# Performance work log

Measured on AMD Instinct MI355X. Metric: run time of the kernel, lower is better.

Reference implementation:

```python
import jax, jax.numpy as jnp
import numpy as np
import math

B, T, C = 2, 8192, 1024
H = 16
HD = C // H  # 64
WIN = 256    # local_window_size


def _rope_tables(T, hd):
    inv_freq = 1.0 / (10000.0 ** (np.arange(0, hd, 2, dtype=np.float32) / hd))
    t = np.arange(T, dtype=np.float32)
    freqs = np.outer(t, inv_freq)                      # [T, hd/2]
    emb = np.concatenate([freqs, freqs], axis=-1)      # [T, hd]
    return jnp.asarray(np.cos(emb))[None, None], jnp.asarray(np.sin(emb))[None, None]


def setup_inputs() -> dict:
    key = jax.random.key(0)
    ks = jax.random.split(key, 10)
    x = jax.random.normal(ks[0], (B, T, C), dtype=jnp.float32)
    # padding_mask: bool [B,T]; per the source, True positions end up masked out of attention
    padding_mask = jax.random.randint(ks[1], (B, T), 0, 2).astype(bool)
    cos, sin = _rope_tables(T, HD)                     # [1,1,T,HD]
    s = 1.0 / math.sqrt(C)
    Wq = jax.random.normal(ks[2], (C, C), dtype=jnp.float32) * s
    bq = jnp.zeros((C,), dtype=jnp.float32)
    Wk = jax.random.normal(ks[3], (C, C), dtype=jnp.float32) * s
    bk = jnp.zeros((C,), dtype=jnp.float32)
    Wv = jax.random.normal(ks[4], (C, C), dtype=jnp.float32) * s
    bv = jnp.zeros((C,), dtype=jnp.float32)
    Wo = jax.random.normal(ks[5], (C, C), dtype=jnp.float32) * s
    bo = jnp.zeros((C,), dtype=jnp.float32)
    return {"x": x, "padding_mask": padding_mask, "cos": cos, "sin": sin,
            "Wq": Wq, "bq": bq, "Wk": Wk, "bk": bk, "Wv": Wv, "bv": bv,
            "Wo": Wo, "bo": bo}


def _rotate_half(t):
    h = t.shape[-1] // 2
    return jnp.concatenate([-t[..., h:], t[..., :h]], axis=-1)


def reference(x, padding_mask, cos, sin, Wq, bq, Wk, bk, Wv, bv, Wo, bo):
    Bx, Tx, Cx = x.shape
    Wn = WIN
    pad_end = (Wn - Tx % Wn) % Wn            # static python int
    Tp = Tx + pad_end
    nW = Tp // Wn
    half = Wn // 2
    hd = cos.shape[-1]

    cos_t = jnp.broadcast_to(cos[0, 0][None], (Bx, Tx, hd))
    sin_t = jnp.broadcast_to(sin[0, 0][None], (Bx, Tx, hd))
    if pad_end > 0:
        x = jnp.pad(x, ((0, 0), (0, pad_end), (0, 0)))
        padding_mask = jnp.pad(padding_mask, ((0, 0), (0, pad_end)))
        cos_t = jnp.pad(cos_t, ((0, 0), (0, pad_end), (0, 0)))
        sin_t = jnp.pad(sin_t, ((0, 0), (0, pad_end), (0, 0)))

    # non-overlapping query windows: [B*nW, W, C]
    q_win = x.reshape(Bx * nW, Wn, Cx)
    cos_q = cos_t.reshape(Bx * nW, Wn, hd)[:, None]   # [Bw,1,W,hd]
    sin_q = sin_t.reshape(Bx * nW, Wn, hd)[:, None]

    # overlapping key/value windows of size 2W, stride W
    x_ctx = jnp.pad(x, ((0, 0), (half, half), (0, 0)))
    cos_ctx = jnp.pad(cos_t, ((0, 0), (half, half), (0, 0)))
    sin_ctx = jnp.pad(sin_t, ((0, 0), (half, half), (0, 0)))
    pk = jnp.pad(padding_mask, ((0, 0), (half, half)))  # pad value False
    idx = jnp.arange(nW)[:, None] * Wn + jnp.arange(2 * Wn)[None, :]  # [nW, 2W]
    k_win = x_ctx[:, idx].reshape(Bx * nW, 2 * Wn, Cx)
    cos_k = cos_ctx[:, idx].reshape(Bx * nW, 2 * Wn, hd)[:, None]
    sin_k = sin_ctx[:, idx].reshape(Bx * nW, 2 * Wn, hd)[:, None]
    pk = pk[:, idx].reshape(Bx * nW, 2 * Wn)

    # attn_mask: True = attend (SDPA bool-mask convention)
    attn_mask = ~pk
    all_attend = jnp.all(attn_mask, axis=-1)
    attn_mask = attn_mask.at[:, 0].set(jnp.where(all_attend, False, attn_mask[:, 0]))

    Bw = Bx * nW
    q = (q_win @ Wq.T + bq).reshape(Bw, Wn, H, HD).transpose(0, 2, 1, 3)        # [Bw,H,W,hd]
    k = (k_win @ Wk.T + bk).reshape(Bw, 2 * Wn, H, HD).transpose(0, 2, 1, 3)    # [Bw,H,2W,hd]
    v = (k_win @ Wv.T + bv).reshape(Bw, 2 * Wn, H, HD).transpose(0, 2, 1, 3)

    q = q * cos_q + _rotate_half(q) * sin_q
    k = k * cos_k + _rotate_half(k) * sin_k

    scale = 1.0 / math.sqrt(HD)
    scores = jnp.einsum('bhqd,bhkd->bhqk', q, k) * scale                        # [Bw,H,W,2W]
    scores = jnp.where(attn_mask[:, None, None, :], scores, jnp.finfo(scores.dtype).min)
    attn = jax.nn.softmax(scores, axis=-1)
    out = jnp.einsum('bhqk,bhkd->bhqd', attn, v)
    out = out.transpose(0, 2, 1, 3).reshape(Bw, Wn, Cx)
    out = out @ Wo.T + bo
    out = out.reshape(Bx, nW * Wn, Cx)[:, :Tx]
    return out
```

## Files before the change

kernel.cpp:

```cpp
#include <hip/hip_runtime.h>
#include <hip/hip_bf16.h>
#include <stdint.h>

#define T_SEQ 8192
#define B_SZ 2
#define CDIM 1024
#define NH 16
#define HDIM 64
#define NW 32

typedef unsigned short ushort_t;
typedef __attribute__((ext_vector_type(8))) short short8;
typedef __attribute__((ext_vector_type(8))) unsigned short us8;
typedef __attribute__((ext_vector_type(4))) unsigned short us4;
typedef __attribute__((ext_vector_type(4))) float f32x4;

__device__ __forceinline__ unsigned short f2bf(float f) {
  union { float f; unsigned int u; } c; c.f = f;
  return (unsigned short)((c.u + 0x7FFFu + ((c.u >> 16) & 1u)) >> 16);
}
__device__ __forceinline__ unsigned pk2(float a, float b) {
  unsigned r;
  asm("v_cvt_pk_bf16_f32 %0, %1, %2" : "=v"(r) : "v"(a), "v"(b));
  return r;
}
__device__ __forceinline__ void gld16(void* lds, const void* g) {
  __builtin_amdgcn_global_load_lds(
      (const __attribute__((address_space(1))) void*)g,
      (__attribute__((address_space(3))) void*)lds, 16, 0, 0);
}

__global__ __launch_bounds__(256) void cvt_f32_bf16(const float* __restrict__ src,
                                                    ushort_t* __restrict__ dst, int n4)
{
  int i = blockIdx.x * 256 + threadIdx.x;
  if (i < n4) {
    float4 v = ((const float4*)src)[i];
    ushort4 o;
    o.x = f2bf(v.x); o.y = f2bf(v.y); o.z = f2bf(v.z); o.w = f2bf(v.w);
    ((ushort4*)dst)[i] = o;
  }
}

__global__ __launch_bounds__(256) void cvt_w4(const float* __restrict__ w0,
                                              const float* __restrict__ w1,
                                              const float* __restrict__ w2,
                                              const float* __restrict__ w3,
                                              ushort_t* __restrict__ dst)
{
  const float* srcs[4] = {w0, w1, w2, w3};
  const float* s = srcs[blockIdx.y];
  ushort_t* d = dst + (size_t)blockIdx.y * CDIM * CDIM;
  int i = blockIdx.x * 256 + threadIdx.x;
  float4 v = ((const float4*)s)[i];
  ushort4 o;
  o.x = f2bf(v.x); o.y = f2bf(v.y); o.z = f2bf(v.z); o.w = f2bf(v.w);
  ((ushort4*)d)[i] = o;
}

__device__ __forceinline__ void gemm_core(const ushort_t* __restrict__ A,
                                          const ushort_t* __restrict__ W,
                                          ushort_t* As, ushort_t* Bs,
                                          int m0, int n0, int t, f32x4 acc[4][4])
{
  const int lane = t & 63;
  const int wv = t >> 6;
  const int wm = (wv >> 1) * 64;
  const int wn = (wv & 1) * 64;
  const int fr = lane & 15;
  const int quad = lane >> 4;

  const int srow = t >> 3;
  const int sc8 = ((t & 7) ^ (srow & 7)) * 8;
  const ushort_t* Ag = A + (size_t)(m0 + srow) * CDIM + sc8;
  const ushort_t* Wg = W + (size_t)(n0 + srow) * CDIM + sc8;
  ushort_t* lA = &As[srow * 64 + (t & 7) * 8];
  ushort_t* lB = &Bs[srow * 64 + (t & 7) * 8];

  for (int kt = 0; kt < CDIM; kt += 64) {
    __syncthreads();
#pragma unroll
    for (int p = 0; p < 4; p++) gld16(lA + p * 2048, Ag + (size_t)p * 32 * CDIM + kt);
#pragma unroll
    for (int p = 0; p < 4; p++) gld16(lB + p * 2048, Wg + (size_t)p * 32 * CDIM + kt);
    __syncthreads();
#pragma unroll
    for (int ks = 0; ks < 2; ks++) {
      short8 a[4], b[4];
#pragma unroll
      for (int i = 0; i < 4; i++)
        a[i] = *(const short8*)&As[(wm + i * 16 + fr) * 64 + (((ks * 4 + quad) ^ (fr & 7)) * 8)];
#pragma unroll
      for (int j = 0; j < 4; j++)
        b[j] = *(const short8*)&Bs[(wn + j * 16 + fr) * 64 + (((ks * 4 + quad) ^ (fr & 7)) * 8)];
#pragma unroll
      for (int i = 0; i < 4; i++)
#pragma unroll
        for (int j = 0; j < 4; j++)
          acc[i][j] = __builtin_amdgcn_mfma_f32_16x16x32_bf16(a[i], b[j], acc[i][j], 0, 0, 0);
    }
  }
}

__global__ __launch_bounds__(256, 4) void gemm_qkv(const ushort_t* __restrict__ A,
                                                   const ushort_t* __restrict__ Wcat,
                                                   const float* __restrict__ bq,
                                                   const float* __restrict__ bk,
                                                   const float* __restrict__ bv,
                                                   ushort_t* __restrict__ Qb,
                                                   ushort_t* __restrict__ Kb,
                                                   ushort_t* __restrict__ Vtb,
                                                   const float* __restrict__ cosT,
                                                   const float* __restrict__ sinT)
{
  __shared__ ushort_t SH[17408];
  ushort_t* As = SH;
  ushort_t* Bs = SH + 8192;

  const int t = threadIdx.x;
  const int lane = t & 63;
  const int wv = t >> 6;
  const int wm = (wv >> 1) * 64;
  const int wn = (wv & 1) * 64;
  const int fr = lane & 15;
  const int quad = lane >> 4;
  const int m0 = blockIdx.y * 128;
  const int n0 = blockIdx.x * 128;
  const int sec = blockIdx.x >> 3;
  const int nsec0 = (blockIdx.x & 7) * 128;
  const float* bias = (sec == 0) ? bq : (sec == 1) ? bk : bv;

  f32x4 acc[4][4];
#pragma unroll
  for (int i = 0; i < 4; i++)
#pragma unroll
    for (int j = 0; j < 4; j++) acc[i][j] = (f32x4){0.f, 0.f, 0.f, 0.f};

  gemm_core(A, Wcat, As, Bs, m0, n0, t, acc);

  __syncthreads();

  if (sec < 2) {
    ushort_t* OutQK = sec ? Kb : Qb;
#pragma unroll
    for (int jp = 0; jp < 2; jp++) {
      int d = jp * 16 + fr;
      int cl = wn + jp * 16 + fr;
      float bl = bias[nsec0 + cl];
      float bh = bias[nsec0 + cl + 32];
#pragma unroll
      for (int i = 0; i < 4; i++) {
        int rloc = wm + i * 16 + quad * 4;
#pragma unroll
        for (int r = 0; r < 4; r++) {
          int tt = (m0 + rloc + r) & (T_SEQ - 1);
          float c = cosT[tt * HDIM + d];
          float sn = sinT[tt * HDIM + d];
          float lo = acc[i][jp][r] + bl;
          float hi = acc[i][jp + 2][r] + bh;
          SH[(rloc + r) * 136 + cl] = f2bf(lo * c - hi * sn);
          SH[(rloc + r) * 136 + cl + 32] = f2bf(hi * c + lo * sn);
        }
      }
    }
    __syncthreads();
    const int rr0 = t >> 4;
    const int c8 = (t & 15) * 8;
    size_t gbase = (size_t)m0 * CDIM + nsec0 + c8;
#pragma unroll
    for (int p = 0; p < 8; p++) {
      int rr = p * 16 + rr0;
      *(us8*)&OutQK[gbase + (size_t)rr * CDIM] = *(const us8*)&SH[rr * 136 + c8];
    }
  } else {
#pragma unroll
    for (int j = 0; j < 4; j++) {
      int ch = nsec0 + wn + j * 16 + fr;
      float bvv = bias[ch];
#pragma unroll
      for (int i = 0; i < 4; i++) {
        int m = m0 + wm + i * 16 + quad * 4;
        int bb = m >> 13;
        int tq = m & (T_SEQ - 1);
        us4 pk;
#pragma unroll
        for (int r = 0; r < 4; r++) pk[r] = f2bf(acc[i][j][r] + bvv);
        *(us4*)&Vtb[((size_t)bb * CDIM + ch) * T_SEQ + tq] = pk;
      }
    }
  }
}

__global__ __launch_bounds__(256, 4) void gemm_out(const ushort_t* __restrict__ A,
                                                   const ushort_t* __restrict__ W,
                                                   const float* __restrict__ bias,
                                                   float* __restrict__ Out)
{
  __shared__ ushort_t SH[16384];
  ushort_t* As = SH;
  ushort_t* Bs = SH + 8192;

  const int t = threadIdx.x;
  const int lane = t & 63;
  const int wv = t >> 6;
  const int wm = (wv >> 1) * 64;
  const int wn = (wv & 1) * 64;
  const int fr = lane & 15;
  const int quad = lane >> 4;
  const int m0 = blockIdx.y * 128;
  const int n0 = blockIdx.x * 128;

  f32x4 acc[4][4];
#pragma unroll
  for (int i = 0; i < 4; i++)
#pragma unroll
    for (int j = 0; j < 4; j++) acc[i][j] = (f32x4){0.f, 0.f, 0.f, 0.f};

  gemm_core(A, W, As, Bs, m0, n0, t, acc);

#pragma unroll
  for (int j = 0; j < 4; j++) {
    int n = n0 + wn + j * 16 + fr;
    float bvv = bias[n];
#pragma unroll
    for (int i = 0; i < 4; i++) {
      int m = m0 + wm + i * 16 + quad * 4;
#pragma unroll
      for (int r = 0; r < 4; r++)
        Out[(size_t)(m + r) * CDIM + n] = acc[i][j][r] + bvv;
    }
  }
}

__global__ __launch_bounds__(256, 4) void attn_kernel(const ushort_t* __restrict__ Q,
                                                      const ushort_t* __restrict__ Kg,
                                                      const ushort_t* __restrict__ Vt,
                                                      const int* __restrict__ mask,
                                                      ushort_t* __restrict__ AO)
{
  __shared__ ushort_t Ks[64 * 72];
  __shared__ ushort_t Vts[64 * 72];
  __shared__ unsigned int PsW[4 * 32 * 32];
  __shared__ float attf[512];

  const int t = threadIdx.x;
  const int lane = t & 63;
  const int wv = t >> 6;
  const int h = blockIdx.x;
  const int w = blockIdx.y >> 1;
  const int qh = blockIdx.y & 1;
  const int b = blockIdx.z;
  const int fr = lane & 15;
  const int quad = lane >> 4;

  {
    int p0 = w * 256 + t - 128;
    bool a0 = (p0 < 0 || p0 >= T_SEQ) ? true : (mask[b * T_SEQ + p0] == 0);
    int p1 = p0 + 256;
    bool a1 = (p1 < 0 || p1 >= T_SEQ) ? true : (mask[b * T_SEQ + p1] == 0);
    int all1 = __syncthreads_and((int)(a0 && a1));
    attf[t] = a0 ? 0.f : -1.0e38f;
    attf[t + 256] = a1 ? 0.f : -1.0e38f;
    if (all1 && t == 0) attf[0] = -1.0e38f;
  }

  short8 qf[2][2];
  {
    const ushort_t* qp = Q + ((size_t)b * T_SEQ + w * 256 + qh * 128 + wv * 32 + fr) * CDIM
                           + h * HDIM + quad * 8;
#pragma unroll
    for (int mt = 0; mt < 2; mt++)
#pragma unroll
      for (int ks = 0; ks < 2; ks++)
        qf[mt][ks] = *(const short8*)&qp[(size_t)mt * 16 * CDIM + ks * 32];
  }

  const int srow = t >> 3;
  const int sc8 = (t & 7) * 8;
  const ushort_t* kgb = Kg + (size_t)b * T_SEQ * CDIM + h * HDIM + sc8;
  const ushort_t* vt_base = Vt + ((size_t)b * CDIM + h * HDIM) * T_SEQ;
  const float SCL = 0.18033688011112042f;

  unsigned int* pw = &PsW[wv * 1024];
  const int swz = (fr & 7) << 2;
  const int rbase = quad << 2;

  float m_run[2], l_run[2];
  f32x4 o[2][4];
#pragma unroll
  for (int mt = 0; mt < 2; mt++) { m_run[mt] = -3.0e38f; l_run[mt] = 0.f; }
#pragma unroll
  for (int mt = 0; mt < 2; mt++)
#pragma unroll
    for (int nt = 0; nt < 4; nt++) o[mt][nt] = (f32x4){0.f, 0.f, 0.f, 0.f};

  for (int kc = 0; kc < 8; kc++) {
    __syncthreads();
    {
#pragma unroll
      for (int p = 0; p < 2; p++) {
        int jj = p * 32 + srow;
        int pos = w * 256 + kc * 64 + jj - 128;
        us8 kval = (us8)(0);
        if (pos >= 0 && pos < T_SEQ) kval = *(const us8*)&kgb[(size_t)pos * CDIM];
        *(us8*)&Ks[jj * 72 + sc8] = kval;
      }
      int pos0 = w * 256 + kc * 64 - 128 + sc8;
      bool inr = (pos0 >= 0) && (pos0 < T_SEQ);
#pragma unroll
      for (int p = 0; p < 2; p++) {
        int d = p * 32 + srow;
        us8 vv = (us8)(0);
        if (inr) vv = *(const us8*)&vt_base[(size_t)d * T_SEQ + pos0];
        *(us8*)&Vts[d * 72 + sc8] = vv;
      }
    }
    __syncthreads();

    short8 kf[4][2];
#pragma unroll
    for (int nt = 0; nt < 4; nt++)
#pragma unroll
      for (int ks = 0; ks < 2; ks++)
        kf[nt][ks] = *(const short8*)&Ks[(nt * 16 + fr) * 72 + ks * 32 + quad * 8];

    f32x4 st[2][4];
#pragma unroll
    for (int mt = 0; mt < 2; mt++)
#pragma unroll
      for (int nt = 0; nt < 4; nt++) {
        f32x4 a = (f32x4){0.f, 0.f, 0.f, 0.f};
        a = __builtin_amdgcn_mfma_f32_16x16x32_bf16(kf[nt][0], qf[mt][0], a, 0, 0, 0);
        a = __builtin_amdgcn_mfma_f32_16x16x32_bf16(kf[nt][1], qf[mt][1], a, 0, 0, 0);
        st[mt][nt] = a;
      }

    f32x4 kb[4];
#pragma unroll
    for (int nt = 0; nt < 4; nt++)
      kb[nt] = *(const f32x4*)&attf[kc * 64 + nt * 16 + quad * 4];
#pragma unroll
    for (int mt = 0; mt < 2; mt++)
#pragma unroll
      for (int nt = 0; nt < 4; nt++)
#pragma unroll
        for (int r = 0; r < 4; r++)
          st[mt][nt][r] = __builtin_fmaf(st[mt][nt][r], SCL, kb[nt][r]);

#pragma unroll
    for (int mt = 0; mt < 2; mt++) {
      float t0 = fmaxf(fmaxf(st[mt][0][0], st[mt][0][1]), fmaxf(st[mt][0][2], st[mt][0][3]));
      float t1 = fmaxf(fmaxf(st[mt][1][0], st[mt][1][1]), fmaxf(st[mt][1][2], st[mt][1][3]));
      float t2 = fmaxf(fmaxf(st[mt][2][0], st[mt][2][1]), fmaxf(st[mt][2][2], st[mt][2][3]));
      float t3 = fmaxf(fmaxf(st[mt][3][0], st[mt][3][1]), fmaxf(st[mt][3][2], st[mt][3][3]));
      float mx = fmaxf(fmaxf(t0, t1), fmaxf(t2, t3));
      mx = fmaxf(mx, __shfl_xor(mx, 16, 64));
      mx = fmaxf(mx, __shfl_xor(mx, 32, 64));
      if (!__all(mx <= m_run[mt] + 8.f)) {
        float mnew = fmaxf(m_run[mt], mx);
        float alpha = __builtin_amdgcn_exp2f(m_run[mt] - mnew);
        m_run[mt] = mnew;
        l_run[mt] *= alpha;
        float af[4];
#pragma unroll
        for (int r = 0; r < 4; r++) af[r] = __shfl(alpha, rbase + r, 64);
#pragma unroll
        for (int nt = 0; nt < 4; nt++)
#pragma unroll
          for (int r = 0; r < 4; r++) o[mt][nt][r] *= af[r];
      }
      float rs = 0.f;
#pragma unroll
      for (int nt = 0; nt < 4; nt++)
#pragma unroll
        for (int r = 0; r < 4; r++) {
          float p = __builtin_amdgcn_exp2f(st[mt][nt][r] - m_run[mt]);
          st[mt][nt][r] = p;
          rs += p;
        }
      rs += __shfl_xor(rs, 16, 64);
      rs += __shfl_xor(rs, 32, 64);
      l_run[mt] += rs;

      unsigned int* pr = pw + ((mt * 16 + fr) << 5);
#pragma unroll
      for (int nt = 0; nt < 4; nt++)
#pragma unroll
        for (int hh = 0; hh < 2; hh++)
          pr[(((nt << 3) + (quad << 1) + hh)) ^ swz] =
              pk2(st[mt][nt][2 * hh], st[mt][nt][2 * hh + 1]);
    }

    short8 vf[4][2];
#pragma unroll
    for (int nt = 0; nt < 4; nt++)
#pragma unroll
      for (int ks = 0; ks < 2; ks++)
        vf[nt][ks] = *(const short8*)&Vts[(nt * 16 + fr) * 72 + ks * 32 + quad * 8];

#pragma unroll
    for (int mt = 0; mt < 2; mt++) {
      const unsigned int* pr = pw + ((mt * 16 + fr) << 5);
      short8 pf[2];
#pragma unroll
      for (int ks = 0; ks < 2; ks++)
        pf[ks] = *(const short8*)&pr[((ks << 4) + (quad << 2)) ^ swz];
#pragma unroll
      for (int nt = 0; nt < 4; nt++) {
        o[mt][nt] = __builtin_amdgcn_mfma_f32_16x16x32_bf16(pf[0], vf[nt][0], o[mt][nt], 0, 0, 0);
        o[mt][nt] = __builtin_amdgcn_mfma_f32_16x16x32_bf16(pf[1], vf[nt][1], o[mt][nt], 0, 0, 0);
      }
    }
  }

  size_t obase = ((size_t)b * T_SEQ + w * 256 + qh * 128 + wv * 32) * CDIM + h * HDIM;
#pragma unroll
  for (int mt = 0; mt < 2; mt++)
#pragma unroll
    for (int r = 0; r < 4; r++) {
      float lv = __shfl(l_run[mt], rbase + r, 64);
      float iv = 1.0f / fmaxf(lv, 1e-30f);
      int row = mt * 16 + quad * 4 + r;
#pragma unroll
      for (int nt = 0; nt < 4; nt++)
        AO[obase + (size_t)row * CDIM + nt * 16 + fr] = f2bf(o[mt][nt][r] * iv);
    }
}

extern "C" void kernel_launch(void* const* d_in, const int* in_sizes, int n_in,
                              void* d_out, int out_size, void* d_ws, size_t ws_size,
                              hipStream_t stream)
{
  const float* x    = (const float*)d_in[0];
  const int*   pm   = (const int*)d_in[1];
  const float* cosT = (const float*)d_in[2];
  const float* sinT = (const float*)d_in[3];
  const float* Wq   = (const float*)d_in[4];
  const float* bq   = (const float*)d_in[5];
  const float* Wk   = (const float*)d_in[6];
  const float* bk   = (const float*)d_in[7];
  const float* Wv   = (const float*)d_in[8];
  const float* bv   = (const float*)d_in[9];
  const float* Wo   = (const float*)d_in[10];
  const float* bo   = (const float*)d_in[11];
  float* out = (float*)d_out;

  const size_t NTOK = (size_t)B_SZ * T_SEQ;
  const size_t NELT = NTOK * CDIM;
  ushort_t* Kb  = (ushort_t*)d_out;
  ushort_t* xbf = (ushort_t*)d_out + NELT;
  char* ws = (char*)d_ws;
  ushort_t* Wbf = (ushort_t*)ws;
  ushort_t* Qb  = (ushort_t*)(ws + 4 * (size_t)CDIM * CDIM * 2);
  ushort_t* Vtb = Qb + NELT;
  ushort_t* AO  = Qb;

  cvt_f32_bf16<<<(int)(NELT / 4 / 256), 256, 0, stream>>>(x, xbf, (int)(NELT / 4));
  cvt_w4<<<dim3(CDIM * CDIM / 4 / 256, 4), 256, 0, stream>>>(Wq, Wk, Wv, Wo, Wbf);

  gemm_qkv<<<dim3(24, (int)(NTOK / 128)), 256, 0, stream>>>(
      xbf, Wbf, bq, bk, bv, Qb, Kb, Vtb, cosT, sinT);

  attn_kernel<<<dim3(NH, NW * 2, B_SZ), 256, 0, stream>>>(Qb, Kb, Vtb, pm, AO);

  gemm_out<<<dim3(8, (int)(NTOK / 128)), 256, 0, stream>>>(
      AO, Wbf + 3 * (size_t)CDIM * CDIM, bo, out);
}
```

Baseline: 420.8 us.

## Use 512-thread attention blocks per window to share K/V tiles across all queries

Each attention block now covers a whole 256-query window with 8 waves instead of splitting it across two 256-thread blocks. This halves the global loads of K/V into shared memory and the mask setup per window, since each thread loads one row instead of two. The P scratch buffer per wave shrinks because P is written and consumed per m-tile, and s_setprio is wrapped around the MFMA sections to favour matrix issue. The change also halves the grid size and raises per-block register and LDS pressure under the new launch bounds.

```diff
diff --git a/kernel.cpp b/kernel.cpp
--- a/kernel.cpp
+++ b/kernel.cpp
@@ -232,7 +232,7 @@
   }
 }
 
-__global__ __launch_bounds__(256, 4) void attn_kernel(const ushort_t* __restrict__ Q,
+__global__ __launch_bounds__(512, 8) void attn_kernel(const ushort_t* __restrict__ Q,
                                                       const ushort_t* __restrict__ Kg,
                                                       const ushort_t* __restrict__ Vt,
                                                       const int* __restrict__ mask,
@@ -240,33 +240,29 @@
 {
   __shared__ ushort_t Ks[64 * 72];
   __shared__ ushort_t Vts[64 * 72];
-  __shared__ unsigned int PsW[4 * 32 * 32];
+  __shared__ unsigned int PsW[8 * 16 * 32];
   __shared__ float attf[512];
 
   const int t = threadIdx.x;
   const int lane = t & 63;
   const int wv = t >> 6;
   const int h = blockIdx.x;
-  const int w = blockIdx.y >> 1;
-  const int qh = blockIdx.y & 1;
+  const int w = blockIdx.y;
   const int b = blockIdx.z;
   const int fr = lane & 15;
   const int quad = lane >> 4;
 
   {
     int p0 = w * 256 + t - 128;
-    bool a0 = (p0 < 0 || p0 >= T_SEQ) ? true : (mask[b * T_SEQ + p0] == 0);
-    int p1 = p0 + 256;
-    bool a1 = (p1 < 0 || p1 >= T_SEQ) ? true : (mask[b * T_SEQ + p1] == 0);
-    int all1 = __syncthreads_and((int)(a0 && a1));
-    attf[t] = a0 ? 0.f : -1.0e38f;
-    attf[t + 256] = a1 ? 0.f : -1.0e38f;
+    bool a = (p0 < 0 || p0 >= T_SEQ) ? true : (mask[b * T_SEQ + p0] == 0);
+    int all1 = __syncthreads_and((int)a);
+    attf[t] = a ? 0.f : -1.0e38f;
     if (all1 && t == 0) attf[0] = -1.0e38f;
   }
 
   short8 qf[2][2];
   {
-    const ushort_t* qp = Q + ((size_t)b * T_SEQ + w * 256 + qh * 128 + wv * 32 + fr) * CDIM
+    const ushort_t* qp = Q + ((size_t)b * T_SEQ + w * 256 + wv * 32 + fr) * CDIM
                            + h * HDIM + quad * 8;
 #pragma unroll
     for (int mt = 0; mt < 2; mt++)
@@ -281,7 +277,7 @@
   const ushort_t* vt_base = Vt + ((size_t)b * CDIM + h * HDIM) * T_SEQ;
   const float SCL = 0.18033688011112042f;
 
-  unsigned int* pw = &PsW[wv * 1024];
+  unsigned int* pw = &PsW[wv * 512];
   const int swz = (fr & 7) << 2;
   const int rbase = quad << 2;
 
@@ -297,23 +293,15 @@
   for (int kc = 0; kc < 8; kc++) {
     __syncthreads();
     {
-#pragma unroll
-      for (int p = 0; p < 2; p++) {
-        int jj = p * 32 + srow;
-        int pos = w * 256 + kc * 64 + jj - 128;
-        us8 kval = (us8)(0);
-        if (pos >= 0 && pos < T_SEQ) kval = *(const us8*)&kgb[(size_t)pos * CDIM];
-        *(us8*)&Ks[jj * 72 + sc8] = kval;
-      }
+      int pos = w * 256 + kc * 64 + srow - 128;
+      us8 kval = (us8)(0);
+      if (pos >= 0 && pos < T_SEQ) kval = *(const us8*)&kgb[(size_t)pos * CDIM];
+      *(us8*)&Ks[srow * 72 + sc8] = kval;
+
       int pos0 = w * 256 + kc * 64 - 128 + sc8;
-      bool inr = (pos0 >= 0) && (pos0 < T_SEQ);
-#pragma unroll
-      for (int p = 0; p < 2; p++) {
-        int d = p * 32 + srow;
-        us8 vv = (us8)(0);
-        if (inr) vv = *(const us8*)&vt_base[(size_t)d * T_SEQ + pos0];
-        *(us8*)&Vts[d * 72 + sc8] = vv;
-      }
+      us8 vv = (us8)(0);
+      if (pos0 >= 0 && pos0 < T_SEQ) vv = *(const us8*)&vt_base[(size_t)srow * T_SEQ + pos0];
+      *(us8*)&Vts[srow * 72 + sc8] = vv;
     }
     __syncthreads();
 
@@ -325,6 +313,7 @@
         kf[nt][ks] = *(const short8*)&Ks[(nt * 16 + fr) * 72 + ks * 32 + quad * 8];
 
     f32x4 st[2][4];
+    __builtin_amdgcn_s_setprio(1);
 #pragma unroll
     for (int mt = 0; mt < 2; mt++)
 #pragma unroll
@@ -334,6 +323,7 @@
         a = __builtin_amdgcn_mfma_f32_16x16x32_bf16(kf[nt][1], qf[mt][1], a, 0, 0, 0);
         st[mt][nt] = a;
       }
+    __builtin_amdgcn_s_setprio(0);
 
     f32x4 kb[4];
 #pragma unroll
@@ -346,6 +336,13 @@
 #pragma unroll
         for (int r = 0; r < 4; r++)
           st[mt][nt][r] = __builtin_fmaf(st[mt][nt][r], SCL, kb[nt][r]);
+
+    short8 vf[4][2];
+#pragma unroll
+    for (int nt = 0; nt < 4; nt++)
+#pragma unroll
+      for (int ks = 0; ks < 2; ks++)
+        vf[nt][ks] = *(const short8*)&Vts[(nt * 16 + fr) * 72 + ks * 32 + quad * 8];
 
 #pragma unroll
     for (int mt = 0; mt < 2; mt++) {
@@ -382,38 +379,30 @@
       rs += __shfl_xor(rs, 32, 64);
       l_run[mt] += rs;
 
-      unsigned int* pr = pw + ((mt * 16 + fr) << 5);
+      unsigned int* pr = pw + (fr << 5);
 #pragma unroll
       for (int nt = 0; nt < 4; nt++)
 #pragma unroll
         for (int hh = 0; hh < 2; hh++)
           pr[(((nt << 3) + (quad << 1) + hh)) ^ swz] =
               pk2(st[mt][nt][2 * hh], st[mt][nt][2 * hh + 1]);
-    }
-
-    short8 vf[4][2];
-#pragma unroll
-    for (int nt = 0; nt < 4; nt++)
-#pragma unroll
-      for (int ks = 0; ks < 2; ks++)
-        vf[nt][ks] = *(const short8*)&Vts[(nt * 16 + fr) * 72 + ks * 32 + quad * 8];
-
-#pragma unroll
-    for (int mt = 0; mt < 2; mt++) {
-      const unsigned int* pr = pw + ((mt * 16 + fr) << 5);
+
       short8 pf[2];
 #pragma unroll
       for (int ks = 0; ks < 2; ks++)
         pf[ks] = *(const short8*)&pr[((ks << 4) + (quad << 2)) ^ swz];
+
+      __builtin_amdgcn_s_setprio(1);
 #pragma unroll
       for (int nt = 0; nt < 4; nt++) {
         o[mt][nt] = __builtin_amdgcn_mfma_f32_16x16x32_bf16(pf[0], vf[nt][0], o[mt][nt], 0, 0, 0);
         o[mt][nt] = __builtin_amdgcn_mfma_f32_16x16x32_bf16(pf[1], vf[nt][1], o[mt][nt], 0, 0, 0);
       }
-    }
-  }
-
-  size_t obase = ((size_t)b * T_SEQ + w * 256 + qh * 128 + wv * 32) * CDIM + h * HDIM;
+      __builtin_amdgcn_s_setprio(0);
+    }
+  }
+
+  size_t obase = ((size_t)b * T_SEQ + w * 256 + wv * 32) * CDIM + h * HDIM;
 #pragma unroll
   for (int mt = 0; mt < 2; mt++)
 #pragma unroll
@@ -461,7 +450,7 @@
   gemm_qkv<<<dim3(24, (int)(NTOK / 128)), 256, 0, stream>>>(
       xbf, Wbf, bq, bk, bv, Qb, Kb, Vtb, cosT, sinT);
 
-  attn_kernel<<<dim3(NH, NW * 2, B_SZ), 256, 0, stream>>>(Qb, Kb, Vtb, pm, AO);
+  attn_kernel<<<dim3(NH, NW, B_SZ), 512, 0, stream>>>(Qb, Kb, Vtb, pm, AO);
 
   gemm_out<<<dim3(8, (int)(NTOK / 128)), 256, 0, stream>>>(
       AO, Wbf + 3 * (size_t)CDIM * CDIM, bo, out);
```

Result: slower. 968.2 us (+130.1%).

## Use 256x256 double-buffered GEMM tiles with XCD swizzle and MFMA priority

Applied to the files above, without the earlier changes.

Both projection GEMMs move from 128x128 tiles with 256 threads to 256x256 tiles with 512 threads. The K loop is double-buffered in 128KB of dynamic LDS, so the next tile's global loads overlap the current MFMAs and one barrier per iteration is dropped. Workgroups are remapped across XCDs for better L2 locality, and s_setprio raises wave priority around MFMA blocks in the GEMM and attention kernels. The cost is one workgroup per CU and fewer total blocks (768 for QKV, 256 for the output GEMM), which may hurt load balance. The QKV epilogue is also split into two serialized halves with extra barriers.

```diff
diff --git a/kernel.cpp b/kernel.cpp
--- a/kernel.cpp
+++ b/kernel.cpp
@@ -58,51 +58,86 @@
   ((ushort4*)d)[i] = o;
 }
 
-__device__ __forceinline__ void gemm_core(const ushort_t* __restrict__ A,
-                                          const ushort_t* __restrict__ W,
-                                          ushort_t* As, ushort_t* Bs,
-                                          int m0, int n0, int t, f32x4 acc[4][4])
+__device__ __forceinline__ void gemm256_core(const ushort_t* __restrict__ A,
+                                             const ushort_t* __restrict__ W,
+                                             ushort_t* SH,
+                                             int m0, int n0, int t, f32x4 acc[8][4])
 {
   const int lane = t & 63;
   const int wv = t >> 6;
-  const int wm = (wv >> 1) * 64;
-  const int wn = (wv & 1) * 64;
+  const int wr = wv >> 2;
+  const int wc = wv & 3;
   const int fr = lane & 15;
   const int quad = lane >> 4;
 
-  const int srow = t >> 3;
-  const int sc8 = ((t & 7) ^ (srow & 7)) * 8;
-  const ushort_t* Ag = A + (size_t)(m0 + srow) * CDIM + sc8;
-  const ushort_t* Wg = W + (size_t)(n0 + srow) * CDIM + sc8;
-  ushort_t* lA = &As[srow * 64 + (t & 7) * 8];
-  ushort_t* lB = &Bs[srow * 64 + (t & 7) * 8];
-
-  for (int kt = 0; kt < CDIM; kt += 64) {
+  ushort_t* As = SH;
+  ushort_t* Bs = SH + 32768;
+
+  const int sr8 = lane >> 3;
+  const int scb = ((lane & 7) ^ sr8) * 8;
+  const int srowb = wv * 8 + sr8;
+  const ushort_t* Ag = A + (size_t)(m0 + srowb) * CDIM + scb;
+  const ushort_t* Wg = W + (size_t)(n0 + srowb) * CDIM + scb;
+  ushort_t* lA = As + srowb * 64 + (lane & 7) * 8;
+  ushort_t* lB = Bs + srowb * 64 + (lane & 7) * 8;
+
+#pragma unroll
+  for (int p = 0; p < 4; p++) {
+    gld16(lA + p * 4096, Ag + (size_t)p * 64 * CDIM);
+    gld16(lB + p * 4096, Wg + (size_t)p * 64 * CDIM);
+  }
+  __syncthreads();
+
+  for (int kt = 0; kt < CDIM / 64; ++kt) {
+    const int cur = kt & 1;
+    if (kt + 1 < CDIM / 64) {
+      const ushort_t* Agn = Ag + (kt + 1) * 64;
+      const ushort_t* Wgn = Wg + (kt + 1) * 64;
+      ushort_t* nA = lA + (cur ^ 1) * 16384;
+      ushort_t* nB = lB + (cur ^ 1) * 16384;
+#pragma unroll
+      for (int p = 0; p < 4; p++) {
+        gld16(nA + p * 4096, Agn + (size_t)p * 64 * CDIM);
+        gld16(nB + p * 4096, Wgn + (size_t)p * 64 * CDIM);
+      }
+    }
+    const ushort_t* Ac = As + cur * 16384;
+    const ushort_t* Bc = Bs + cur * 16384;
+    short8 b[4][2];
+#pragma unroll
+    for (int j = 0; j < 4; j++)
+#pragma unroll
+      for (int ks = 0; ks < 2; ks++)
+        b[j][ks] = *(const short8*)&Bc[(wc * 64 + j * 16 + fr) * 64 +
+                                       (((ks * 4 + quad) ^ (fr & 7)) * 8)];
+    __builtin_amdgcn_s_setprio(1);
+#pragma unroll
+    for (int i = 0; i < 8; i++) {
+      const int ra = (wr * 128 + i * 16 + fr) * 64;
+      short8 a0 = *(const short8*)&Ac[ra + ((quad ^ (fr & 7)) * 8)];
+      short8 a1 = *(const short8*)&Ac[ra + (((4 + quad) ^ (fr & 7)) * 8)];
+#pragma unroll
+      for (int j = 0; j < 4; j++)
+        acc[i][j] = __builtin_amdgcn_mfma_f32_16x16x32_bf16(a0, b[j][0], acc[i][j], 0, 0, 0);
+#pragma unroll
+      for (int j = 0; j < 4; j++)
+        acc[i][j] = __builtin_amdgcn_mfma_f32_16x16x32_bf16(a1, b[j][1], acc[i][j], 0, 0, 0);
+    }
+    __builtin_amdgcn_s_setprio(0);
     __syncthreads();
-#pragma unroll
-    for (int p = 0; p < 4; p++) gld16(lA + p * 2048, Ag + (size_t)p * 32 * CDIM + kt);
-#pragma unroll
-    for (int p = 0; p < 4; p++) gld16(lB + p * 2048, Wg + (size_t)p * 32 * CDIM + kt);
-    __syncthreads();
-#pragma unroll
-    for (int ks = 0; ks < 2; ks++) {
-      short8 a[4], b[4];
-#pragma unroll
-      for (int i = 0; i < 4; i++)
-        a[i] = *(const short8*)&As[(wm + i * 16 + fr) * 64 + (((ks * 4 + quad) ^ (fr & 7)) * 8)];
-#pragma unroll
-      for (int j = 0; j < 4; j++)
-        b[j] = *(const short8*)&Bs[(wn + j * 16 + fr) * 64 + (((ks * 4 + quad) ^ (fr & 7)) * 8)];
-#pragma unroll
-      for (int i = 0; i < 4; i++)
-#pragma unroll
-        for (int j = 0; j < 4; j++)
-          acc[i][j] = __builtin_amdgcn_mfma_f32_16x16x32_bf16(a[i], b[j], acc[i][j], 0, 0, 0);
-    }
-  }
-}
-
-__global__ __launch_bounds__(256, 4) void gemm_qkv(const ushort_t* __restrict__ A,
+  }
+}
+
+__device__ __forceinline__ void xcd_swz(int& bx, int& by) {
+  int gx = gridDim.x, nwg = gx * gridDim.y;
+  int lid = bx + gx * by;
+  int cpx = nwg >> 3;
+  int swz = (lid & 7) * cpx + (lid >> 3);
+  bx = swz % gx;
+  by = swz / gx;
+}
+
+__global__ __launch_bounds__(512, 1) void gemm_qkv(const ushort_t* __restrict__ A,
                                                    const ushort_t* __restrict__ Wcat,
                                                    const float* __restrict__ bq,
                                                    const float* __restrict__ bk,
@@ -113,73 +148,78 @@
                                                    const float* __restrict__ cosT,
                                                    const float* __restrict__ sinT)
 {
-  __shared__ ushort_t SH[17408];
-  ushort_t* As = SH;
-  ushort_t* Bs = SH + 8192;
+  extern __shared__ ushort_t SH[];
 
   const int t = threadIdx.x;
   const int lane = t & 63;
   const int wv = t >> 6;
-  const int wm = (wv >> 1) * 64;
-  const int wn = (wv & 1) * 64;
+  const int wr = wv >> 2;
+  const int wc = wv & 3;
   const int fr = lane & 15;
   const int quad = lane >> 4;
-  const int m0 = blockIdx.y * 128;
-  const int n0 = blockIdx.x * 128;
-  const int sec = blockIdx.x >> 3;
-  const int nsec0 = (blockIdx.x & 7) * 128;
+  int bx = blockIdx.x, by = blockIdx.y;
+  xcd_swz(bx, by);
+  const int m0 = by * 256;
+  const int n0 = bx * 256;
+  const int sec = bx >> 2;
+  const int nsec0 = (bx & 3) * 256;
   const float* bias = (sec == 0) ? bq : (sec == 1) ? bk : bv;
 
-  f32x4 acc[4][4];
-#pragma unroll
-  for (int i = 0; i < 4; i++)
+  f32x4 acc[8][4];
+#pragma unroll
+  for (int i = 0; i < 8; i++)
 #pragma unroll
     for (int j = 0; j < 4; j++) acc[i][j] = (f32x4){0.f, 0.f, 0.f, 0.f};
 
-  gemm_core(A, Wcat, As, Bs, m0, n0, t, acc);
-
-  __syncthreads();
+  gemm256_core(A, Wcat, SH, m0, n0, t, acc);
 
   if (sec < 2) {
     ushort_t* OutQK = sec ? Kb : Qb;
 #pragma unroll
-    for (int jp = 0; jp < 2; jp++) {
-      int d = jp * 16 + fr;
-      int cl = wn + jp * 16 + fr;
-      float bl = bias[nsec0 + cl];
-      float bh = bias[nsec0 + cl + 32];
-#pragma unroll
-      for (int i = 0; i < 4; i++) {
-        int rloc = wm + i * 16 + quad * 4;
-#pragma unroll
-        for (int r = 0; r < 4; r++) {
-          int tt = (m0 + rloc + r) & (T_SEQ - 1);
-          float c = cosT[tt * HDIM + d];
-          float sn = sinT[tt * HDIM + d];
-          float lo = acc[i][jp][r] + bl;
-          float hi = acc[i][jp + 2][r] + bh;
-          SH[(rloc + r) * 136 + cl] = f2bf(lo * c - hi * sn);
-          SH[(rloc + r) * 136 + cl + 32] = f2bf(hi * c + lo * sn);
+    for (int half = 0; half < 2; ++half) {
+      if (wr == half) {
+#pragma unroll
+        for (int jp = 0; jp < 2; jp++) {
+          int d = jp * 16 + fr;
+          int cl = wc * 64 + jp * 16 + fr;
+          float bl = bias[nsec0 + cl];
+          float bh = bias[nsec0 + cl + 32];
+#pragma unroll
+          for (int i = 0; i < 8; i++) {
+            int rloc = i * 16 + quad * 4;
+#pragma unroll
+            for (int r = 0; r < 4; r++) {
+              int m = m0 + half * 128 + rloc + r;
+              int tt = m & (T_SEQ - 1);
+              float c = cosT[tt * HDIM + d];
+              float sn = sinT[tt * HDIM + d];
+              float lo = acc[i][jp][r] + bl;
+              float hi = acc[i][jp + 2][r] + bh;
+              SH[(rloc + r) * 264 + cl] = f2bf(lo * c - hi * sn);
+              SH[(rloc + r) * 264 + cl + 32] = f2bf(hi * c + lo * sn);
+            }
+          }
         }
       }
-    }
-    __syncthreads();
-    const int rr0 = t >> 4;
-    const int c8 = (t & 15) * 8;
-    size_t gbase = (size_t)m0 * CDIM + nsec0 + c8;
-#pragma unroll
-    for (int p = 0; p < 8; p++) {
-      int rr = p * 16 + rr0;
-      *(us8*)&OutQK[gbase + (size_t)rr * CDIM] = *(const us8*)&SH[rr * 136 + c8];
+      __syncthreads();
+      const int rr0 = t >> 5;
+      const int c8 = (t & 31) * 8;
+      size_t gbase = (size_t)(m0 + half * 128) * CDIM + nsec0 + c8;
+#pragma unroll
+      for (int pp = 0; pp < 8; pp++) {
+        int rr = pp * 16 + rr0;
+        *(us8*)&OutQK[gbase + (size_t)rr * CDIM] = *(const us8*)&SH[rr * 264 + c8];
+      }
+      __syncthreads();
     }
   } else {
 #pragma unroll
     for (int j = 0; j < 4; j++) {
-      int ch = nsec0 + wn + j * 16 + fr;
+      int ch = nsec0 + wc * 64 + j * 16 + fr;
       float bvv = bias[ch];
 #pragma unroll
-      for (int i = 0; i < 4; i++) {
-        int m = m0 + wm + i * 16 + quad * 4;
+      for (int i = 0; i < 8; i++) {
+        int m = m0 + wr * 128 + i * 16 + quad * 4;
         int bb = m >> 13;
         int tq = m & (T_SEQ - 1);
         us4 pk;
@@ -191,40 +231,40 @@
   }
 }
 
-__global__ __launch_bounds__(256, 4) void gemm_out(const ushort_t* __restrict__ A,
+__global__ __launch_bounds__(512, 1) void gemm_out(const ushort_t* __restrict__ A,
                                                    const ushort_t* __restrict__ W,
                                                    const float* __restrict__ bias,
                                                    float* __restrict__ Out)
 {
-  __shared__ ushort_t SH[16384];
-  ushort_t* As = SH;
-  ushort_t* Bs = SH + 8192;
+  extern __shared__ ushort_t SH[];
 
   const int t = threadIdx.x;
   const int lane = t & 63;
   const int wv = t >> 6;
-  const int wm = (wv >> 1) * 64;
-  const int wn = (wv & 1) * 64;
+  const int wr = wv >> 2;
+  const int wc = wv & 3;
   const int fr = lane & 15;
   const int quad = lane >> 4;
-  const int m0 = blockIdx.y * 128;
-  const int n0 = blockIdx.x * 128;
-
-  f32x4 acc[4][4];
-#pragma unroll
-  for (int i = 0; i < 4; i++)
+  int bx = blockIdx.x, by = blockIdx.y;
+  xcd_swz(bx, by);
+  const int m0 = by * 256;
+  const int n0 = bx * 256;
+
+  f32x4 acc[8][4];
+#pragma unroll
+  for (int i = 0; i < 8; i++)
 #pragma unroll
     for (int j = 0; j < 4; j++) acc[i][j] = (f32x4){0.f, 0.f, 0.f, 0.f};
 
-  gemm_core(A, W, As, Bs, m0, n0, t, acc);
+  gemm256_core(A, W, SH, m0, n0, t, acc);
 
 #pragma unroll
   for (int j = 0; j < 4; j++) {
-    int n = n0 + wn + j * 16 + fr;
+    int n = n0 + wc * 64 + j * 16 + fr;
     float bvv = bias[n];
 #pragma unroll
-    for (int i = 0; i < 4; i++) {
-      int m = m0 + wm + i * 16 + quad * 4;
+    for (int i = 0; i < 8; i++) {
+      int m = m0 + wr * 128 + i * 16 + quad * 4;
 #pragma unroll
       for (int r = 0; r < 4; r++)
         Out[(size_t)(m + r) * CDIM + n] = acc[i][j][r] + bvv;
@@ -325,6 +365,7 @@
         kf[nt][ks] = *(const short8*)&Ks[(nt * 16 + fr) * 72 + ks * 32 + quad * 8];
 
     f32x4 st[2][4];
+    __builtin_amdgcn_s_setprio(1);
 #pragma unroll
     for (int mt = 0; mt < 2; mt++)
 #pragma unroll
@@ -334,6 +375,7 @@
         a = __builtin_amdgcn_mfma_f32_16x16x32_bf16(kf[nt][1], qf[mt][1], a, 0, 0, 0);
         st[mt][nt] = a;
       }
+    __builtin_amdgcn_s_setprio(0);
 
     f32x4 kb[4];
 #pragma unroll
@@ -398,6 +440,7 @@
       for (int ks = 0; ks < 2; ks++)
         vf[nt][ks] = *(const short8*)&Vts[(nt * 16 + fr) * 72 + ks * 32 + quad * 8];
 
+    __builtin_amdgcn_s_setprio(1);
 #pragma unroll
     for (int mt = 0; mt < 2; mt++) {
       const unsigned int* pr = pw + ((mt * 16 + fr) << 5);
@@ -411,6 +454,7 @@
         o[mt][nt] = __builtin_amdgcn_mfma_f32_16x16x32_bf16(pf[1], vf[nt][1], o[mt][nt], 0, 0, 0);
       }
     }
+    __builtin_amdgcn_s_setprio(0);
   }
 
   size_t obase = ((size_t)b * T_SEQ + w * 256 + qh * 128 + wv * 32) * CDIM + h * HDIM;
@@ -445,6 +489,15 @@
   const float* bo   = (const float*)d_in[11];
   float* out = (float*)d_out;
 
+  static bool attr_done = false;
+  if (!attr_done) {
+    hipFuncSetAttribute(reinterpret_cast<const void*>(gemm_qkv),
+                        hipFuncAttributeMaxDynamicSharedMemorySize, 131072);
+    hipFuncSetAttribute(reinterpret_cast<const void*>(gemm_out),
+                        hipFuncAttributeMaxDynamicSharedMemorySize, 131072);
+    attr_done = true;
+  }
+
   const size_t NTOK = (size_t)B_SZ * T_SEQ;
   const size_t NELT = NTOK * CDIM;
   ushort_t* Kb  = (ushort_t*)d_out;
@@ -458,11 +511,11 @@
   cvt_f32_bf16<<<(int)(NELT / 4 / 256), 256, 0, stream>>>(x, xbf, (int)(NELT / 4));
   cvt_w4<<<dim3(CDIM * CDIM / 4 / 256, 4), 256, 0, stream>>>(Wq, Wk, Wv, Wo, Wbf);
 
-  gemm_qkv<<<dim3(24, (int)(NTOK / 128)), 256, 0, stream>>>(
+  gemm_qkv<<<dim3(12, (int)(NTOK / 256)), 512, 131072, stream>>>(
       xbf, Wbf, bq, bk, bv, Qb, Kb, Vtb, cosT, sinT);
 
   attn_kernel<<<dim3(NH, NW * 2, B_SZ), 256, 0, stream>>>(Qb, Kb, Vtb, pm, AO);
 
-  gemm_out<<<dim3(8, (int)(NTOK / 128)), 256, 0, stream>>>(
+  gemm_out<<<dim3(4, (int)(NTOK / 256)), 512, 131072, stream>>>(
       AO, Wbf + 3 * (size_t)CDIM * CDIM, bo, out);
 }
```

New measurement: 406.8 us. 1.03x faster.
